# Optimization experiments

Hardware: AMD Instinct MI355X
Metric: run time of the kernel (lower is better)

The kernel has to match this reference:

```python
import jax, jax.numpy as jnp
import numpy as np

R = 16       # voxel resolution
CH = 64      # channels
NSAMPLE = 16
PROJ = 3


def _bn(x, p, eps):
    # p: [4, C] rows = (gamma, beta, running_mean, running_var); eval-mode BN
    g, b, m, v = p
    sh = [1] * x.ndim
    sh[1] = -1
    return (x - m.reshape(sh)) * (g.reshape(sh) * jax.lax.rsqrt(v.reshape(sh) + eps)) + b.reshape(sh)


def _gather_ch(x, flat_idx):
    # x: [B, C, M], flat_idx: [B, L] -> [B, C, L]
    B, C, _ = x.shape
    idx = jnp.broadcast_to(flat_idx[:, None, :], (B, C, flat_idx.shape[1]))
    return jnp.take_along_axis(x, idx, axis=2)


def _pvb_forward(x, xyz, idx, w3d1, b3d1, bn3d1, w3d2, b3d2, bn3d2, proj_w1, proj_bn, proj_w2, pt_bn):
    B, C, N = x.shape
    r = R
    # ---------- voxelization (coords detached, normalize=False) ----------
    nc = xyz - xyz.mean(axis=2, keepdims=True)
    nc = jnp.clip((nc + 1.0) * 0.5 * r, 0.0, r - 1.0)
    nc = jax.lax.stop_gradient(nc)                        # [B,3,N] float in [0, r-1]
    vi = jnp.round(nc).astype(jnp.int32)
    flat = (vi[:, 0] * r + vi[:, 1]) * r + vi[:, 2]       # [B,N]
    seg = (flat + jnp.arange(B, dtype=jnp.int32)[:, None] * (r ** 3)).reshape(-1)
    feats = x.transpose(0, 2, 1).reshape(B * N, C)
    sums = jax.ops.segment_sum(feats, seg, num_segments=B * r ** 3)
    cnts = jax.ops.segment_sum(jnp.ones((B * N,), x.dtype), seg, num_segments=B * r ** 3)
    v = (sums / jnp.maximum(cnts, 1.0)[:, None]).reshape(B, r, r, r, C).transpose(0, 4, 1, 2, 3)
    # ---------- depthwise Conv3d -> BN3d -> LeakyReLU (x2) ----------
    dn = ('NCDHW', 'OIDHW', 'NCDHW')
    v = jax.lax.conv_general_dilated(v, w3d1, (1, 1, 1), 'SAME', dimension_numbers=dn,
                                     feature_group_count=C) + b3d1.reshape(1, C, 1, 1, 1)
    v = jax.nn.leaky_relu(_bn(v, bn3d1, 1e-4), 0.1)
    v = jax.lax.conv_general_dilated(v, w3d2, (1, 1, 1), 'SAME', dimension_numbers=dn,
                                     feature_group_count=C) + b3d2.reshape(1, C, 1, 1, 1)
    v = jax.nn.leaky_relu(_bn(v, bn3d2, 1e-4), 0.1)
    # ---------- trilinear devoxelize ----------
    vf = v.reshape(B, C, r ** 3)
    lo = jnp.floor(nc).astype(jnp.int32)
    fr = nc - lo
    hi = jnp.minimum(lo + 1, r - 1)
    p_v_x = jnp.zeros((B, C, N), x.dtype)
    for dx in (0, 1):
        for dy in (0, 1):
            for dz in (0, 1):
                xi = hi[:, 0] if dx else lo[:, 0]
                yi = hi[:, 1] if dy else lo[:, 1]
                zi = hi[:, 2] if dz else lo[:, 2]
                w = ((fr[:, 0] if dx else 1.0 - fr[:, 0]) *
                     (fr[:, 1] if dy else 1.0 - fr[:, 1]) *
                     (fr[:, 2] if dz else 1.0 - fr[:, 2]))
                p_v_x = p_v_x + w[:, None, :] * _gather_ch(vf, (xi * r + yi) * r + zi)
    # ---------- neighbor gather (precomputed ball-query idx) ----------
    K = idx.shape[-1]
    flat_nb = idx.reshape(B, N * K)
    x_j = _gather_ch(x, flat_nb).reshape(B, C, N, K)
    xyz_j = _gather_ch(xyz, flat_nb).reshape(B, 3, N, K)
    dp1 = xyz_j - xyz[:, :, :, None]                      # [B,3,N,K]
    df = x_j - x[:, :, :, None]                           # [B,C,N,K]
    # proj_conv: 1x1 conv -> BN2d -> ReLU -> 1x1 conv
    h = jnp.einsum('oc,bcnk->bonk', proj_w1, df)
    h = jax.nn.relu(_bn(h, proj_bn, 1e-5))
    dp2 = jnp.einsum('oc,bcnk->bonk', proj_w2, h)         # [B,3,N,K]
    dp = jnp.concatenate([dp1, dp2], axis=1)              # [B,6,N,K]
    # repeat_interleave of the 6 channels up to C (last gets remainder)
    part = 6
    rep = C // part
    repeats = np.array([rep] * (part - 1) + [C - rep * (part - 1)])
    w = jnp.repeat(dp, repeats, axis=1, total_repeat_length=C)
    x_j = x_j * w
    x_j = jax.nn.relu(_bn(x_j, pt_bn, 1e-5))              # proj_transform
    p_p_x = x_j.max(axis=-1)                              # max-pool over neighbors
    return p_v_x + p_p_x                                  # agg_way == 'add'


def setup_inputs() -> dict:
    key = jax.random.key(0)
    ks = jax.random.split(key, 16)
    B, C, N, K = 4, CH, 16384, NSAMPLE

    def bn_params(k, c):
        k1, k2, k3, k4 = jax.random.split(k, 4)
        return jnp.stack([1.0 + 0.1 * jax.random.normal(k1, (c,), jnp.float32),
                          0.1 * jax.random.normal(k2, (c,), jnp.float32),
                          0.1 * jax.random.normal(k3, (c,), jnp.float32),
                          jax.random.uniform(k4, (c,), jnp.float32, 0.5, 1.5)])

    return dict(
        x=jax.random.normal(ks[0], (B, C, N), jnp.float32),
        xyz=jax.random.uniform(ks[1], (B, 3, N), jnp.float32, -1.0, 1.0),
        idx=jax.random.randint(ks[2], (B, N, K), 0, N, jnp.int32),
        w3d1=0.1 * jax.random.normal(ks[3], (C, 1, 3, 3, 3), jnp.float32),
        b3d1=0.01 * jax.random.normal(ks[4], (C,), jnp.float32),
        bn3d1=bn_params(ks[5], C),
        w3d2=0.1 * jax.random.normal(ks[6], (C, 1, 3, 3, 3), jnp.float32),
        b3d2=0.01 * jax.random.normal(ks[7], (C,), jnp.float32),
        bn3d2=bn_params(ks[8], C),
        proj_w1=0.1 * jax.random.normal(ks[9], (PROJ, C), jnp.float32),
        proj_bn=bn_params(ks[10], PROJ),
        proj_w2=0.3 * jax.random.normal(ks[11], (PROJ, PROJ), jnp.float32),
        pt_bn=bn_params(ks[12], C),
    )


def reference(x, xyz, idx, w3d1, b3d1, bn3d1, w3d2, b3d2, bn3d2, proj_w1, proj_bn, proj_w2, pt_bn):
    return _pvb_forward(x, xyz, idx, w3d1, b3d1, bn3d1, w3d2, b3d2, bn3d2, proj_w1, proj_bn, proj_w2, pt_bn)
```

## Files before the change

kernel.cpp:

```cpp
#include <hip/hip_runtime.h>

namespace {
constexpr int B_  = 4;
constexpr int C_  = 64;
constexpr int N_  = 16384;
constexpr int K_  = 16;
constexpr int R3_ = 4096;

constexpr int OFF_MEANS = 0;
constexpr int OFF_XT    = 16;
constexpr int OFF_PTS   = OFF_XT   + B_*N_*C_/2;
constexpr int OFF_PTSH  = OFF_PTS  + B_*N_*8;
constexpr int OFF_DVT   = OFF_PTSH + B_*N_*4;
constexpr int OFF_SUMS  = OFF_DVT  + B_*N_*8;
constexpr int OFF_CNTS  = OFF_SUMS + B_*R3_*C_;
constexpr int OFF_VT16  = OFF_CNTS + B_*R3_;
constexpr int FILL_FLOATS = B_*R3_*C_ + B_*R3_;
constexpr int FILL_BLOCKS = FILL_FLOATS / (256 * 4);
}

__device__ __forceinline__ unsigned short f2bf(float f) {
  unsigned u = __float_as_uint(f);
  return (unsigned short)((u + 0x7FFFu + ((u >> 16) & 1u)) >> 16);
}
__device__ __forceinline__ float bf2f(unsigned short h) {
  return __uint_as_float(((unsigned)h) << 16);
}
__device__ __forceinline__ unsigned cvtpk_bf16(float lo, float hi) {
  unsigned r;
  asm("v_cvt_pk_bf16_f32 %0, %1, %2" : "=v"(r) : "v"(lo), "v"(hi));
  return r;
}
__device__ __forceinline__ float bflo(unsigned u) { return __uint_as_float(u << 16); }
__device__ __forceinline__ float bfhi(unsigned u) { return __uint_as_float(u & 0xffff0000u); }

__global__ __launch_bounds__(256) void k_init(
    const float* __restrict__ xyz, float* __restrict__ means,
    float* __restrict__ fill) {
  const int blk = blockIdx.x;
  if (blk >= 12) {
    const int base = (blk - 12) * (256 * 4) + threadIdx.x * 4;
    *(float4*)(fill + base) = make_float4(0.f, 0.f, 0.f, 0.f);
    return;
  }
  __shared__ double red[256];
  const float* p = xyz + blk * N_;
  double s = 0.0;
  for (int i = threadIdx.x; i < N_; i += 256) s += (double)p[i];
  red[threadIdx.x] = s;
  __syncthreads();
  for (int st = 128; st; st >>= 1) {
    if (threadIdx.x < st) red[threadIdx.x] += red[threadIdx.x + st];
    __syncthreads();
  }
  if (threadIdx.x == 0) means[blk] = (float)(red[0] * (1.0 / (double)N_));
}

__global__ __launch_bounds__(256) void k_prep(
    const float* __restrict__ x, const float* __restrict__ xyz,
    const float* __restrict__ pw1, const float* __restrict__ means,
    unsigned short* __restrict__ xT, float* __restrict__ pts,
    unsigned* __restrict__ ptsh, unsigned* __restrict__ dvt,
    float* __restrict__ sums, float* __restrict__ cnts) {
  __shared__ float tile[64 * 65];
  __shared__ float ncs[3][64];
  __shared__ float xys[3][64];
  __shared__ float hps[3][64];
  __shared__ int   flats[64];

  const int t   = threadIdx.x;
  const int blk = blockIdx.x;
  const int b   = blk >> 8;
  const int n0  = (blk & 255) << 6;

#pragma unroll
  for (int i = 0; i < 4; ++i) {
    int c = i * 16 + (t >> 4);
    int j4 = (t & 15) * 4;
    float4 v = *(const float4*)&x[((size_t)(b * C_ + c)) * N_ + n0 + j4];
    tile[c * 65 + j4 + 0] = v.x;
    tile[c * 65 + j4 + 1] = v.y;
    tile[c * 65 + j4 + 2] = v.z;
    tile[c * 65 + j4 + 3] = v.w;
  }
  __syncthreads();

  unsigned* __restrict__ xT32 = (unsigned*)xT;
#pragma unroll
  for (int i = 0; i < 8; ++i) {
    int p = i * 8 + (t >> 5);
    int c2 = (t & 31) * 2;
    unsigned pk = cvtpk_bf16(tile[c2 * 65 + p], tile[(c2 + 1) * 65 + p]);
    xT32[((size_t)(b * N_ + n0 + p)) * 32 + (t & 31)] = pk;
  }

  if (t < 192) {
    int p = t & 63, q = t >> 6;
    float s = 0.f;
#pragma unroll
    for (int c = 0; c < 64; ++c) s = fmaf(pw1[q * 64 + c], tile[c * 65 + p], s);
    size_t pb = ((size_t)(b * N_ + n0 + p)) * 8;
    pts[pb + 3 + q] = s;
    hps[q][p] = s;
    float v = xyz[((size_t)(b * 3 + q)) * N_ + n0 + p];
    pts[pb + q] = v;
    xys[q][p] = v;
    float nc = fminf(fmaxf((v - means[b * 3 + q] + 1.0f) * 8.0f, 0.0f), 15.0f);
    ncs[q][p] = nc;
  } else {
    int p = t & 63;
    size_t pb = ((size_t)(b * N_ + n0 + p)) * 8;
    pts[pb + 6] = 0.f;
    pts[pb + 7] = 0.f;
  }
  __syncthreads();

  if (t < 64) {
    const float nc0 = ncs[0][t], nc1 = ncs[1][t], nc2 = ncs[2][t];
    int vx = (int)rintf(nc0);
    int vy = (int)rintf(nc1);
    int vz = (int)rintf(nc2);
    int f = (vx * 16 + vy) * 16 + vz;
    flats[t] = f;
    atomicAdd(&cnts[b * R3_ + f], 1.0f);
    uint4 r;
    r.x = cvtpk_bf16(xys[0][t], xys[1][t]);
    r.y = cvtpk_bf16(xys[2][t], hps[0][t]);
    r.z = cvtpk_bf16(hps[1][t], hps[2][t]);
    r.w = 0u;
    *(uint4*)&ptsh[((size_t)(b * N_ + n0 + t)) * 4] = r;
    int lx = (int)nc0, ly = (int)nc1, lz = (int)nc2;
    float fx = nc0 - (float)lx, fy = nc1 - (float)ly, fz = nc2 - (float)lz;
    int hx = lx < 15 ? lx + 1 : 15;
    int hy = ly < 15 ? ly + 1 : 15;
    int hz = lz < 15 ? lz + 1 : 15;
    float wx[2] = {1.f - fx, fx};
    float wy[2] = {1.f - fy, fy};
    float wz[2] = {1.f - fz, fz};
    int xi[2] = {lx, hx}, yi[2] = {ly, hy}, zi[2] = {lz, hz};
    unsigned c8v[8];
#pragma unroll
    for (int c8 = 0; c8 < 8; ++c8) {
      int dx = c8 >> 2, dy = (c8 >> 1) & 1, dz = c8 & 1;
      int flat = (xi[dx] * 16 + yi[dy]) * 16 + zi[dz];
      float wt = wx[dx] * wy[dy] * wz[dz];
      c8v[c8] = ((unsigned)flat << 16) | (unsigned)f2bf(wt);
    }
    unsigned* dp = dvt + ((size_t)(b * N_ + n0 + t)) * 8;
    *(uint4*)dp       = make_uint4(c8v[0], c8v[1], c8v[2], c8v[3]);
    *(uint4*)(dp + 4) = make_uint4(c8v[4], c8v[5], c8v[6], c8v[7]);
  }
  __syncthreads();

  const int w = t >> 6, lane = t & 63;
#pragma unroll
  for (int i = 0; i < 16; ++i) {
    int p = w * 16 + i;
    int f = flats[p];
    atomicAdd(&sums[((size_t)(b * R3_ + f)) * C_ + lane], tile[lane * 65 + p]);
  }
}

__global__ __launch_bounds__(256) void k_tr(
    const float* __restrict__ sums, const float* __restrict__ cnts,
    unsigned* __restrict__ vT16) {
  __shared__ float tile[64 * 65];
  __shared__ float rs[64];
  const int t = threadIdx.x;
  const int b = blockIdx.x >> 6;
  const int v0 = (blockIdx.x & 63) << 6;

#pragma unroll
  for (int i = 0; i < 16; ++i) {
    int r = i * 4 + (t >> 6);
    int c = t & 63;
    tile[r * 65 + c] = sums[((size_t)(b * R3_ + v0 + r)) * C_ + c];
  }
  if (t < 64) rs[t] = 1.0f / fmaxf(cnts[b * R3_ + v0 + t], 1.0f);
  __syncthreads();

#pragma unroll
  for (int i = 0; i < 8; ++i) {
    int d = t + i * 256;
    int c = d >> 5, vp = (d & 31) * 2;
    unsigned pk = cvtpk_bf16(tile[vp * 65 + c] * rs[vp],
                             tile[(vp + 1) * 65 + c] * rs[vp + 1]);
    vT16[((size_t)(b * C_ + c)) * 2048 + (v0 >> 1) + (d & 31)] = pk;
  }
}

__global__ __launch_bounds__(256, 8) void k_point(
    const unsigned short* __restrict__ xT, const float* __restrict__ pts,
    const unsigned* __restrict__ ptsh, const int* __restrict__ idx,
    const float* __restrict__ pbn, const float* __restrict__ pw2,
    const float* __restrict__ ptbn, float* __restrict__ out) {
  __shared__ unsigned w6[3][513];
  __shared__ int      jarr[512];
  __shared__ float    outT[64 * 33];

  const int t = threadIdx.x;
  const int blk = blockIdx.x;
  const int xcd = blk & 7;
  const int b = xcd >> 1;
  const int t32 = ((blk >> 3) << 1) | (xcd & 1);
  const int n0 = t32 * 32;

  const float psc0 = pbn[0] * rsqrtf(pbn[9]  + 1e-5f);
  const float psc1 = pbn[1] * rsqrtf(pbn[10] + 1e-5f);
  const float psc2 = pbn[2] * rsqrtf(pbn[11] + 1e-5f);
  const float pof0 = pbn[3] - pbn[6] * psc0;
  const float pof1 = pbn[4] - pbn[7] * psc1;
  const float pof2 = pbn[5] - pbn[8] * psc2;
  float W2r[9];
#pragma unroll
  for (int i = 0; i < 9; ++i) W2r[i] = pw2[i];

  const float* __restrict__ ptsb = pts + (size_t)b * N_ * 8;
  const unsigned* __restrict__ ptshb = ptsh + (size_t)b * N_ * 4;

#pragma unroll
  for (int rep = 0; rep < 2; ++rep) {
    const int q = t + rep * 256;
    const int p = q >> 4;
    const int n = n0 + p;
    const int j = idx[(size_t)b * N_ * K_ + (size_t)n0 * K_ + q];
    jarr[q] = j;
    uint4 q4 = *(const uint4*)(ptshb + (size_t)j * 4);
    const float qx0 = bflo(q4.x), qx1 = bfhi(q4.x);
    const float qx2 = bflo(q4.y), qh0 = bfhi(q4.y);
    const float qh1 = bflo(q4.z), qh2 = bfhi(q4.z);
    const float* ir = ptsb + (size_t)n * 8;
    float4 pa = *(const float4*)ir;
    float4 pb = *(const float4*)(ir + 4);
    float d0 = qx0 - pa.x, d1 = qx1 - pa.y, d2 = qx2 - pa.z;
    float c0 = pof0 - psc0 * pa.w;
    float c1 = pof1 - psc1 * pb.x;
    float c2 = pof2 - psc2 * pb.y;
    float h0 = fmaxf(fmaf(qh0, psc0, c0), 0.f);
    float h1 = fmaxf(fmaf(qh1, psc1, c1), 0.f);
    float h2 = fmaxf(fmaf(qh2, psc2, c2), 0.f);
    float e0 = fmaf(W2r[0], h0, fmaf(W2r[1], h1, W2r[2] * h2));
    float e1 = fmaf(W2r[3], h0, fmaf(W2r[4], h1, W2r[5] * h2));
    float e2 = fmaf(W2r[6], h0, fmaf(W2r[7], h1, W2r[8] * h2));
    w6[0][q] = cvtpk_bf16(d0, d1);
    w6[1][q] = cvtpk_bf16(d2, e0);
    w6[2][q] = cvtpk_bf16(e1, e2);
  }
  __syncthreads();

  const int w = t >> 6, lane = t & 63;
  const int widx = lane < 20 ? 0 : lane < 40 ? 1 : 2;
  const bool hi = (lane >= 10 && lane < 20) || (lane >= 30 && lane < 40) || (lane >= 50);
  const unsigned shl = hi ? 0u : 16u;
  const float ts = ptbn[lane] * rsqrtf(ptbn[192 + lane] + 1e-5f);
  const float td = ptbn[64 + lane] - ptbn[128 + lane] * ts;
  const unsigned short* __restrict__ xTb = xT + (size_t)b * N_ * C_;

#pragma unroll
  for (int i = 0; i < 8; ++i) {
    const int p = i * 4 + w;
    const int pq = p * 16;

    unsigned short xjv[16];
#pragma unroll
    for (int k = 0; k < 16; ++k)
      xjv[k] = xTb[(size_t)jarr[pq + k] * C_ + lane];

    float pm = 0.f;
#pragma unroll
    for (int k = 0; k < 16; ++k) {
      float wf = __uint_as_float(w6[widx][pq + k] << shl);
      pm = fmaxf(pm, fmaf(bf2f(xjv[k]) * wf, ts, td));
    }

    outT[lane * 33 + p] = pm;
  }
  __syncthreads();

#pragma unroll
  for (int i = 0; i < 8; ++i) {
    int c = i * 8 + (t >> 5);
    int col = t & 31;
    out[((size_t)(b * C_ + c)) * N_ + n0 + col] = outT[c * 33 + col];
  }
}

__global__ __launch_bounds__(256) void k_convdevox(
    const unsigned* __restrict__ vT16,
    const float* __restrict__ w3d1, const float* __restrict__ b3d1,
    const float* __restrict__ bn1, const float* __restrict__ w3d2,
    const float* __restrict__ b3d2, const float* __restrict__ bn2,
    const unsigned* __restrict__ dvt, float* __restrict__ out) {
  __shared__ float va[18 * 18 * 20];
  __shared__ float vb[18 * 18 * 20];
  __shared__ float vls[R3_];
  const int t = threadIdx.x;
  const int b = blockIdx.x >> 6;
  const int c = blockIdx.x & 63;

  float W1[27], W2[27];
#pragma unroll
  for (int i = 0; i < 27; ++i) { W1[i] = w3d1[c * 27 + i]; W2[i] = w3d2[c * 27 + i]; }
  const float s1 = bn1[c] / sqrtf(bn1[192 + c] + 1e-4f);
  const float d1 = (b3d1[c] - bn1[128 + c]) * s1 + bn1[64 + c];
  const float s2 = bn2[c] / sqrtf(bn2[192 + c] + 1e-4f);
  const float d2 = (b3d2[c] - bn2[128 + c]) * s2 + bn2[64 + c];

  for (int i = t; i < 18 * 18 * 20; i += 256) { va[i] = 0.f; vb[i] = 0.f; }
  const unsigned* __restrict__ vrow = vT16 + ((size_t)(b * C_ + c)) * 2048;
  __syncthreads();

#pragma unroll
  for (int i = 0; i < 8; ++i) {
    int d = t + i * 256;
    unsigned u = vrow[d];
    int vox0 = d * 2;
    int z = vox0 & 15, y = (vox0 >> 4) & 15, xx = vox0 >> 8;
    int base = ((xx + 1) * 18 + (y + 1)) * 20 + (z + 1);
    va[base]     = bflo(u);
    va[base + 1] = bfhi(u);
  }
  __syncthreads();

  const int x = t >> 4, y = t & 15;
  float acc[16];

#pragma unroll
  for (int z = 0; z < 16; ++z) acc[z] = 0.f;
#pragma unroll
  for (int dx = 0; dx < 3; ++dx)
#pragma unroll
    for (int dy = 0; dy < 3; ++dy) {
      const float* row = &va[((x + dx) * 18 + (y + dy)) * 20];
      float wv[18];
      *(float4*)&wv[0]  = *(const float4*)&row[0];
      *(float4*)&wv[4]  = *(const float4*)&row[4];
      *(float4*)&wv[8]  = *(const float4*)&row[8];
      *(float4*)&wv[12] = *(const float4*)&row[12];
      wv[16] = row[16]; wv[17] = row[17];
      const float k0 = W1[(dx * 3 + dy) * 3 + 0];
      const float k1 = W1[(dx * 3 + dy) * 3 + 1];
      const float k2 = W1[(dx * 3 + dy) * 3 + 2];
#pragma unroll
      for (int z = 0; z < 16; ++z)
        acc[z] = fmaf(k0, wv[z], fmaf(k1, wv[z + 1], fmaf(k2, wv[z + 2], acc[z])));
    }
  {
    const int wb = ((x + 1) * 18 + (y + 1)) * 20 + 1;
#pragma unroll
    for (int z = 0; z < 16; ++z) {
      float tt = acc[z] * s1 + d1;
      vb[wb + z] = tt > 0.f ? tt : 0.1f * tt;
    }
  }
  __syncthreads();

#pragma unroll
  for (int z = 0; z < 16; ++z) acc[z] = 0.f;
#pragma unroll
  for (int dx = 0; dx < 3; ++dx)
#pragma unroll
    for (int dy = 0; dy < 3; ++dy) {
      const float* row = &vb[((x + dx) * 18 + (y + dy)) * 20];
      float wv[18];
      *(float4*)&wv[0]  = *(const float4*)&row[0];
      *(float4*)&wv[4]  = *(const float4*)&row[4];
      *(float4*)&wv[8]  = *(const float4*)&row[8];
      *(float4*)&wv[12] = *(const float4*)&row[12];
      wv[16] = row[16]; wv[17] = row[17];
      const float k0 = W2[(dx * 3 + dy) * 3 + 0];
      const float k1 = W2[(dx * 3 + dy) * 3 + 1];
      const float k2 = W2[(dx * 3 + dy) * 3 + 2];
#pragma unroll
      for (int z = 0; z < 16; ++z)
        acc[z] = fmaf(k0, wv[z], fmaf(k1, wv[z + 1], fmaf(k2, wv[z + 2], acc[z])));
    }
  {
    const int vbase = (x * 16 + y) * 16;
#pragma unroll
    for (int z = 0; z < 16; ++z) {
      float tt = acc[z] * s2 + d2;
      vls[vbase + z] = tt > 0.f ? tt : 0.1f * tt;
    }
  }
  __syncthreads();

  const uint4* __restrict__ dv4 = (const uint4*)(dvt + (size_t)b * N_ * 8);
  float* __restrict__ orow = out + ((size_t)(b * C_ + c)) * N_;
#pragma unroll 4
  for (int i = 0; i < 64; ++i) {
    const int n = t + i * 256;
    uint4 a = dv4[n * 2];
    uint4 bq = dv4[n * 2 + 1];
    float o = orow[n];
    float dacc;
    dacc = bflo(a.x)  * vls[a.x  >> 16];
    dacc = fmaf(bflo(a.y),  vls[a.y  >> 16], dacc);
    dacc = fmaf(bflo(a.z),  vls[a.z  >> 16], dacc);
    dacc = fmaf(bflo(a.w),  vls[a.w  >> 16], dacc);
    dacc = fmaf(bflo(bq.x), vls[bq.x >> 16], dacc);
    dacc = fmaf(bflo(bq.y), vls[bq.y >> 16], dacc);
    dacc = fmaf(bflo(bq.z), vls[bq.z >> 16], dacc);
    dacc = fmaf(bflo(bq.w), vls[bq.w >> 16], dacc);
    orow[n] = o + dacc;
  }
}

extern "C" void kernel_launch(void* const* d_in, const int* in_sizes, int n_in,
                              void* d_out, int out_size, void* d_ws, size_t ws_size,
                              hipStream_t stream) {
  const float* x     = (const float*)d_in[0];
  const float* xyz   = (const float*)d_in[1];
  const int*   idx   = (const int*)  d_in[2];
  const float* w3d1  = (const float*)d_in[3];
  const float* b3d1  = (const float*)d_in[4];
  const float* bn3d1 = (const float*)d_in[5];
  const float* w3d2  = (const float*)d_in[6];
  const float* b3d2  = (const float*)d_in[7];
  const float* bn3d2 = (const float*)d_in[8];
  const float* pw1   = (const float*)d_in[9];
  const float* pbn   = (const float*)d_in[10];
  const float* pw2   = (const float*)d_in[11];
  const float* ptbn  = (const float*)d_in[12];
  float* out = (float*)d_out;
  float* ws  = (float*)d_ws;

  k_init<<<dim3(12 + FILL_BLOCKS), dim3(256), 0, stream>>>(
      xyz, ws + OFF_MEANS, ws + OFF_SUMS);
  k_prep<<<dim3(B_ * N_ / 64), dim3(256), 0, stream>>>(
      x, xyz, pw1, ws + OFF_MEANS, (unsigned short*)(ws + OFF_XT), ws + OFF_PTS,
      (unsigned*)(ws + OFF_PTSH), (unsigned*)(ws + OFF_DVT),
      ws + OFF_SUMS, ws + OFF_CNTS);
  k_tr<<<dim3(B_ * 64), dim3(256), 0, stream>>>(
      ws + OFF_SUMS, ws + OFF_CNTS, (unsigned*)(ws + OFF_VT16));
  k_point<<<dim3(B_ * N_ / 32), dim3(256), 0, stream>>>(
      (const unsigned short*)(ws + OFF_XT), ws + OFF_PTS,
      (const unsigned*)(ws + OFF_PTSH), idx, pbn, pw2, ptbn, out);
  k_convdevox<<<dim3(B_ * C_), dim3(256), 0, stream>>>(
      (const unsigned*)(ws + OFF_VT16), w3d1, b3d1, bn3d1, w3d2, b3d2, bn3d2,
      (const unsigned*)(ws + OFF_DVT), out);
}
```

Baseline: 90.88 us.

## Compact devoxelization records to base index plus fractions; use 512-thread conv blocks

```diff
diff --git a/kernel.cpp b/kernel.cpp
--- a/kernel.cpp
+++ b/kernel.cpp
@@ -131,24 +131,10 @@
     *(uint4*)&ptsh[((size_t)(b * N_ + n0 + t)) * 4] = r;
     int lx = (int)nc0, ly = (int)nc1, lz = (int)nc2;
     float fx = nc0 - (float)lx, fy = nc1 - (float)ly, fz = nc2 - (float)lz;
-    int hx = lx < 15 ? lx + 1 : 15;
-    int hy = ly < 15 ? ly + 1 : 15;
-    int hz = lz < 15 ? lz + 1 : 15;
-    float wx[2] = {1.f - fx, fx};
-    float wy[2] = {1.f - fy, fy};
-    float wz[2] = {1.f - fz, fz};
-    int xi[2] = {lx, hx}, yi[2] = {ly, hy}, zi[2] = {lz, hz};
-    unsigned c8v[8];
-#pragma unroll
-    for (int c8 = 0; c8 < 8; ++c8) {
-      int dx = c8 >> 2, dy = (c8 >> 1) & 1, dz = c8 & 1;
-      int flat = (xi[dx] * 16 + yi[dy]) * 16 + zi[dz];
-      float wt = wx[dx] * wy[dy] * wz[dz];
-      c8v[c8] = ((unsigned)flat << 16) | (unsigned)f2bf(wt);
-    }
-    unsigned* dp = dvt + ((size_t)(b * N_ + n0 + t)) * 8;
-    *(uint4*)dp       = make_uint4(c8v[0], c8v[1], c8v[2], c8v[3]);
-    *(uint4*)(dp + 4) = make_uint4(c8v[4], c8v[5], c8v[6], c8v[7]);
+    unsigned base = (unsigned)((lx * 16 + ly) * 16 + lz);
+    unsigned w0 = base | (((unsigned)f2bf(fz)) << 16);
+    unsigned w1 = cvtpk_bf16(fx, fy);
+    *(uint2*)&dvt[((size_t)(b * N_ + n0 + t)) * 2] = make_uint2(w0, w1);
   }
   __syncthreads();
 
@@ -285,7 +271,7 @@
   }
 }
 
-__global__ __launch_bounds__(256) void k_convdevox(
+__global__ __launch_bounds__(512) void k_convdevox(
     const unsigned* __restrict__ vT16,
     const float* __restrict__ w3d1, const float* __restrict__ b3d1,
     const float* __restrict__ bn1, const float* __restrict__ w3d2,
@@ -293,7 +279,7 @@
     const unsigned* __restrict__ dvt, float* __restrict__ out) {
   __shared__ float va[18 * 18 * 20];
   __shared__ float vb[18 * 18 * 20];
-  __shared__ float vls[R3_];
+  __shared__ float vls[4370];
   const int t = threadIdx.x;
   const int b = blockIdx.x >> 6;
   const int c = blockIdx.x & 63;
@@ -306,49 +292,48 @@
   const float s2 = bn2[c] / sqrtf(bn2[192 + c] + 1e-4f);
   const float d2 = (b3d2[c] - bn2[128 + c]) * s2 + bn2[64 + c];
 
-  for (int i = t; i < 18 * 18 * 20; i += 256) { va[i] = 0.f; vb[i] = 0.f; }
+  for (int i = t; i < 18 * 18 * 20; i += 512) { va[i] = 0.f; vb[i] = 0.f; }
+  if (t < 274) vls[4096 + t] = 0.f;
   const unsigned* __restrict__ vrow = vT16 + ((size_t)(b * C_ + c)) * 2048;
   __syncthreads();
 
 #pragma unroll
-  for (int i = 0; i < 8; ++i) {
-    int d = t + i * 256;
+  for (int i = 0; i < 4; ++i) {
+    int d = t + i * 512;
     unsigned u = vrow[d];
     int vox0 = d * 2;
-    int z = vox0 & 15, y = (vox0 >> 4) & 15, xx = vox0 >> 8;
-    int base = ((xx + 1) * 18 + (y + 1)) * 20 + (z + 1);
+    int z = vox0 & 15, yy = (vox0 >> 4) & 15, xx = vox0 >> 8;
+    int base = ((xx + 1) * 18 + (yy + 1)) * 20 + (z + 1);
     va[base]     = bflo(u);
     va[base + 1] = bfhi(u);
   }
   __syncthreads();
 
-  const int x = t >> 4, y = t & 15;
-  float acc[16];
-
-#pragma unroll
-  for (int z = 0; z < 16; ++z) acc[z] = 0.f;
+  const int x = t >> 5, y = (t >> 1) & 15, z0 = (t & 1) * 8;
+  float acc[8];
+
+#pragma unroll
+  for (int z = 0; z < 8; ++z) acc[z] = 0.f;
 #pragma unroll
   for (int dx = 0; dx < 3; ++dx)
 #pragma unroll
     for (int dy = 0; dy < 3; ++dy) {
-      const float* row = &va[((x + dx) * 18 + (y + dy)) * 20];
-      float wv[18];
-      *(float4*)&wv[0]  = *(const float4*)&row[0];
-      *(float4*)&wv[4]  = *(const float4*)&row[4];
-      *(float4*)&wv[8]  = *(const float4*)&row[8];
-      *(float4*)&wv[12] = *(const float4*)&row[12];
-      wv[16] = row[16]; wv[17] = row[17];
+      const float* row = &va[((x + dx) * 18 + (y + dy)) * 20 + z0];
+      float wv[12];
+      *(float4*)&wv[0] = *(const float4*)&row[0];
+      *(float4*)&wv[4] = *(const float4*)&row[4];
+      *(float4*)&wv[8] = *(const float4*)&row[8];
       const float k0 = W1[(dx * 3 + dy) * 3 + 0];
       const float k1 = W1[(dx * 3 + dy) * 3 + 1];
       const float k2 = W1[(dx * 3 + dy) * 3 + 2];
 #pragma unroll
-      for (int z = 0; z < 16; ++z)
+      for (int z = 0; z < 8; ++z)
         acc[z] = fmaf(k0, wv[z], fmaf(k1, wv[z + 1], fmaf(k2, wv[z + 2], acc[z])));
     }
   {
-    const int wb = ((x + 1) * 18 + (y + 1)) * 20 + 1;
-#pragma unroll
-    for (int z = 0; z < 16; ++z) {
+    const int wb = ((x + 1) * 18 + (y + 1)) * 20 + 1 + z0;
+#pragma unroll
+    for (int z = 0; z < 8; ++z) {
       float tt = acc[z] * s1 + d1;
       vb[wb + z] = tt > 0.f ? tt : 0.1f * tt;
     }
@@ -356,53 +341,55 @@
   __syncthreads();
 
 #pragma unroll
-  for (int z = 0; z < 16; ++z) acc[z] = 0.f;
+  for (int z = 0; z < 8; ++z) acc[z] = 0.f;
 #pragma unroll
   for (int dx = 0; dx < 3; ++dx)
 #pragma unroll
     for (int dy = 0; dy < 3; ++dy) {
-      const float* row = &vb[((x + dx) * 18 + (y + dy)) * 20];
-      float wv[18];
-      *(float4*)&wv[0]  = *(const float4*)&row[0];
-      *(float4*)&wv[4]  = *(const float4*)&row[4];
-      *(float4*)&wv[8]  = *(const float4*)&row[8];
-      *(float4*)&wv[12] = *(const float4*)&row[12];
-      wv[16] = row[16]; wv[17] = row[17];
+      const float* row = &vb[((x + dx) * 18 + (y + dy)) * 20 + z0];
+      float wv[12];
+      *(float4*)&wv[0] = *(const float4*)&row[0];
+      *(float4*)&wv[4] = *(const float4*)&row[4];
+      *(float4*)&wv[8] = *(const float4*)&row[8];
       const float k0 = W2[(dx * 3 + dy) * 3 + 0];
       const float k1 = W2[(dx * 3 + dy) * 3 + 1];
       const float k2 = W2[(dx * 3 + dy) * 3 + 2];
 #pragma unroll
-      for (int z = 0; z < 16; ++z)
+      for (int z = 0; z < 8; ++z)
         acc[z] = fmaf(k0, wv[z], fmaf(k1, wv[z + 1], fmaf(k2, wv[z + 2], acc[z])));
     }
   {
-    const int vbase = (x * 16 + y) * 16;
-#pragma unroll
-    for (int z = 0; z < 16; ++z) {
+    const int vbase = (x * 16 + y) * 16 + z0;
+#pragma unroll
+    for (int z = 0; z < 8; ++z) {
       float tt = acc[z] * s2 + d2;
       vls[vbase + z] = tt > 0.f ? tt : 0.1f * tt;
     }
   }
   __syncthreads();
 
-  const uint4* __restrict__ dv4 = (const uint4*)(dvt + (size_t)b * N_ * 8);
+  const uint2* __restrict__ dv2 = (const uint2*)(dvt + (size_t)b * N_ * 2);
   float* __restrict__ orow = out + ((size_t)(b * C_ + c)) * N_;
 #pragma unroll 4
-  for (int i = 0; i < 64; ++i) {
-    const int n = t + i * 256;
-    uint4 a = dv4[n * 2];
-    uint4 bq = dv4[n * 2 + 1];
+  for (int i = 0; i < 32; ++i) {
+    const int n = t + i * 512;
+    uint2 r = dv2[n];
     float o = orow[n];
-    float dacc;
-    dacc = bflo(a.x)  * vls[a.x  >> 16];
-    dacc = fmaf(bflo(a.y),  vls[a.y  >> 16], dacc);
-    dacc = fmaf(bflo(a.z),  vls[a.z  >> 16], dacc);
-    dacc = fmaf(bflo(a.w),  vls[a.w  >> 16], dacc);
-    dacc = fmaf(bflo(bq.x), vls[bq.x >> 16], dacc);
-    dacc = fmaf(bflo(bq.y), vls[bq.y >> 16], dacc);
-    dacc = fmaf(bflo(bq.z), vls[bq.z >> 16], dacc);
-    dacc = fmaf(bflo(bq.w), vls[bq.w >> 16], dacc);
-    orow[n] = o + dacc;
+    const int base = (int)(r.x & 0xffffu);
+    const float fz = bfhi(r.x);
+    const float fx = bflo(r.y), fy = bfhi(r.y);
+    const float* v0 = &vls[base];
+    float a0 = v0[0],   a1 = v0[1];
+    float b0 = v0[16],  b1 = v0[17];
+    float c0 = v0[256], c1 = v0[257];
+    float d0 = v0[272], d1 = v0[273];
+    float zA = fmaf(fz, a1 - a0, a0);
+    float zB = fmaf(fz, b1 - b0, b0);
+    float zC = fmaf(fz, c1 - c0, c0);
+    float zD = fmaf(fz, d1 - d0, d0);
+    float yAB = fmaf(fy, zB - zA, zA);
+    float yCD = fmaf(fy, zD - zC, zC);
+    orow[n] = o + fmaf(fx, yCD - yAB, yAB);
   }
 }
 
@@ -436,7 +423,7 @@
   k_point<<<dim3(B_ * N_ / 32), dim3(256), 0, stream>>>(
       (const unsigned short*)(ws + OFF_XT), ws + OFF_PTS,
       (const unsigned*)(ws + OFF_PTSH), idx, pbn, pw2, ptbn, out);
-  k_convdevox<<<dim3(B_ * C_), dim3(256), 0, stream>>>(
+  k_convdevox<<<dim3(B_ * C_), dim3(512), 0, stream>>>(
       (const unsigned*)(ws + OFF_VT16), w3d1, b3d1, bn3d1, w3d2, b3d2, bn3d2,
       (const unsigned*)(ws + OFF_DVT), out);
 }
```

After: 85.64 us. -5.8%, faster.
